# Kernel tuning notes

Measured on AMD Instinct MI355X. Metric: run time of the kernel, lower is better.

Reference implementation:

```python
import jax, jax.numpy as jnp
import numpy as np

B, H, W, C, NH, WS, NB = 8, 64, 64, 384, 12, 8, 2
N = H * W
NWT = WS * WS  # tokens per window
SHIFT = WS // 2

def _rel_index(ws):
    coords = np.stack(np.meshgrid(np.arange(ws), np.arange(ws), indexing='ij')).reshape(2, -1)
    rel = (coords[:, :, None] - coords[:, None, :]).transpose(1, 2, 0)
    rel[..., 0] += ws - 1
    rel[..., 1] += ws - 1
    rel[..., 0] *= 2 * ws - 1
    return rel.sum(-1)  # (ws*ws, ws*ws)

REL_IDX = _rel_index(WS)

def _shift_mask(h, w, ws, shift):
    img = np.zeros((h, w))
    cnt = 0
    for hs in (slice(0, -ws), slice(-ws, -shift), slice(-shift, None)):
        for wsl in (slice(0, -ws), slice(-ws, -shift), slice(-shift, None)):
            img[hs, wsl] = cnt
            cnt += 1
    win = img.reshape(h // ws, ws, w // ws, ws).transpose(0, 2, 1, 3).reshape(-1, ws * ws)
    diff = win[:, None, :] - win[:, :, None]
    return np.where(diff != 0, -100.0, 0.0).astype(np.float32)  # (nW, NWT, NWT)

MASK = jnp.asarray(_shift_mask(H, W, WS, SHIFT))

def _ln(x, g, b, eps=1e-5):
    m = jnp.mean(x, -1, keepdims=True)
    v = jnp.mean((x - m) ** 2, -1, keepdims=True)
    return (x - m) * jax.lax.rsqrt(v + eps) * g + b

def _partition(x):
    b = x.shape[0]
    x = x.reshape(b, H // WS, WS, W // WS, WS, C).transpose(0, 1, 3, 2, 4, 5)
    return x.reshape(-1, NWT, C)

def _reverse(wx, b):
    x = wx.reshape(b, H // WS, W // WS, WS, WS, C).transpose(0, 1, 3, 2, 4, 5)
    return x.reshape(b, H, W, C)

def _attention(xw, qkv_w, qkv_b, proj_w, proj_b, rpb, mask):
    B_, Nt, Cc = xw.shape
    hd = Cc // NH
    qkv = (xw @ qkv_w + qkv_b).reshape(B_, Nt, 3, NH, hd).transpose(2, 0, 3, 1, 4)
    q, k, v = qkv[0], qkv[1], qkv[2]
    bias = rpb[REL_IDX].transpose(2, 0, 1)[None]  # (1, NH, Nt, Nt)
    attn = jnp.einsum('bhnd,bhmd->bhnm', q * (hd ** -0.5), k) + bias
    if mask is not None:
        nW = mask.shape[0]
        attn = attn.reshape(B_ // nW, nW, NH, Nt, Nt) + mask[None, :, None]
        attn = attn.reshape(B_, NH, Nt, Nt)
    attn = jax.nn.softmax(attn, axis=-1)
    out = jnp.einsum('bhnm,bhmd->bhnd', attn, v).transpose(0, 2, 1, 3).reshape(B_, Nt, Cc)
    return out @ proj_w + proj_b

def _swin_block(x, p, shift):
    n1g, n1b, n2g, n2b, qw, qb, pw, pb, w1, b1, w2, b2, rpb = p
    shortcut = x
    h = _ln(x, n1g, n1b)
    if shift > 0:
        h = jnp.roll(h, (-shift, -shift), axis=(1, 2))
    hw = _attention(_partition(h), qw, qb, pw, pb, rpb, MASK if shift > 0 else None)
    h = _reverse(hw, x.shape[0])
    if shift > 0:
        h = jnp.roll(h, (shift, shift), axis=(1, 2))
    x = shortcut + h
    h = _ln(x, n2g, n2b)
    h = jax.nn.gelu(h @ w1 + b1) @ w2 + b2
    return x + h


def setup_inputs() -> dict:
    key = jax.random.key(0)
    ks = jax.random.split(key, 6)
    s = 0.02
    return {
        'x': jax.random.normal(ks[0], (B, N, C), jnp.float32),
        'outer_g': jnp.ones((NB, C), jnp.float32),
        'outer_b': jnp.zeros((NB, C), jnp.float32),
        'n1_g': jnp.ones((NB, C), jnp.float32),
        'n1_b': jnp.zeros((NB, C), jnp.float32),
        'n2_g': jnp.ones((NB, C), jnp.float32),
        'n2_b': jnp.zeros((NB, C), jnp.float32),
        'qkv_w': jax.random.normal(ks[1], (NB, C, 3 * C), jnp.float32) * s,
        'qkv_b': jnp.zeros((NB, 3 * C), jnp.float32),
        'proj_w': jax.random.normal(ks[2], (NB, C, C), jnp.float32) * s,
        'proj_b': jnp.zeros((NB, C), jnp.float32),
        'mlp_w1': jax.random.normal(ks[3], (NB, C, 4 * C), jnp.float32) * s,
        'mlp_b1': jnp.zeros((NB, 4 * C), jnp.float32),
        'mlp_w2': jax.random.normal(ks[4], (NB, 4 * C, C), jnp.float32) * s,
        'mlp_b2': jnp.zeros((NB, C), jnp.float32),
        'rpb': jax.random.normal(ks[5], (NB, (2 * WS - 1) ** 2, NH), jnp.float32) * s,
    }


def reference(x, outer_g, outer_b, n1_g, n1_b, n2_g, n2_b, qkv_w, qkv_b, proj_w, proj_b, mlp_w1, mlp_b1, mlp_w2, mlp_b2, rpb):
    xv = x.reshape(B, H, W, C)
    for i in range(NB):
        shift = 0 if i % 2 == 0 else SHIFT
        p = (n1_g[i], n1_b[i], n2_g[i], n2_b[i], qkv_w[i], qkv_b[i], proj_w[i], proj_b[i],
             mlp_w1[i], mlp_b1[i], mlp_w2[i], mlp_b2[i], rpb[i])
        residual = xv
        xv = _swin_block(_ln(xv, outer_g[i], outer_b[i]), p, shift) + residual
    return xv.reshape(B, N, C)
```

## Files before the change

kernel.cpp:

```cpp
#include <hip/hip_runtime.h>
#include <hip/hip_bf16.h>

#define BATCH 8
#define HDIM 64
#define WDIM 64
#define CC 384
#define NHE 12
#define HD 32
#define NTOK 32768
#define NBLK 2

typedef short short8 __attribute__((ext_vector_type(8)));
typedef float f32x4 __attribute__((ext_vector_type(4)));

__device__ __forceinline__ float bf2f(unsigned short u) {
  return __uint_as_float(((unsigned int)u) << 16);
}
__device__ __forceinline__ unsigned short f2bf(float f) {
  __hip_bfloat16 h = __float2bfloat16(f);
  return *reinterpret_cast<unsigned short*>(&h);
}
__device__ __forceinline__ float wave_sum(float s) {
#pragma unroll
  for (int o = 32; o; o >>= 1) s += __shfl_xor(s, o, 64);
  return s;
}
__device__ __forceinline__ float gelu_f(float x) {
  float y = 0.7978845608028654f * (x + 0.044715f * x * x * x);
  float t = 1.0f - 2.0f / (__expf(2.0f * y) + 1.0f);
  return 0.5f * x * (1.0f + t);
}
__device__ __forceinline__ int regid(int x) {
  return x < 56 ? 0 : (x < 60 ? 1 : 2);
}
__device__ __forceinline__ void gload16(const void* g, void* l) {
  __builtin_amdgcn_global_load_lds(
      (const __attribute__((address_space(1))) unsigned int*)g,
      (__attribute__((address_space(3))) unsigned int*)l, 16, 0, 0);
}

__global__ __launch_bounds__(256) void wconv_all_kernel(
    const float* __restrict__ qkvw, const float* __restrict__ pw,
    const float* __restrict__ w1, const float* __restrict__ w2,
    unsigned short* __restrict__ wt) {
  int t = blockIdx.x;
  const int i = t / 432;
  t -= i * 432;
  unsigned short* wq = wt + (size_t)i * 1769472;
  const float* src;
  unsigned short* dst;
  int K, N, nx;
  if (t < 108)      { src = qkvw + (size_t)i * 442368; dst = wq;           K = 384;  N = 1152; nx = 18; }
  else if (t < 144) { t -= 108; src = pw + (size_t)i * 147456; dst = wq + 442368;  K = 384;  N = 384;  nx = 6; }
  else if (t < 288) { t -= 144; src = w1 + (size_t)i * 589824; dst = wq + 589824;  K = 384;  N = 1536; nx = 24; }
  else              { t -= 288; src = w2 + (size_t)i * 589824; dst = wq + 1179648; K = 1536; N = 384;  nx = 6; }
  const int bn = (t % nx) * 64, bk = (t / nx) * 64;
  __shared__ float tile[64 * 65];
  const int tt = threadIdx.x;
  const int lk = tt >> 2, ln = (tt & 3) * 16;
  const float* ps = src + (size_t)(bk + lk) * N + bn + ln;
#pragma unroll
  for (int j = 0; j < 4; ++j)
    *(float4*)&tile[lk * 65 + ln + 4 * j] = *(const float4*)(ps + 4 * j);
  __syncthreads();
  const int on = tt >> 2, ok = (tt & 3) * 16;
  unsigned short ob[16];
#pragma unroll
  for (int j = 0; j < 16; ++j) ob[j] = f2bf(tile[(ok + j) * 65 + on]);
  uint4* pd = (uint4*)(dst + (size_t)(bn + on) * K + bk + ok);
  pd[0] = ((const uint4*)ob)[0];
  pd[1] = ((const uint4*)ob)[1];
}

__global__ __launch_bounds__(256) void bias_prep_kernel(
    const float* __restrict__ rpb, float* __restrict__ biasT) {
  int idx = blockIdx.x * 256 + threadIdx.x;
  int m = idx & 63;
  int n = (idx >> 6) & 63;
  int h = idx >> 12;
  int dr = (n >> 3) - (m >> 3) + 7;
  int dc = (n & 7) - (m & 7) + 7;
  biasT[idx] = rpb[(dr * 15 + dc) * NHE + h];
}

__global__ __launch_bounds__(256) void ln_fused_kernel(
    const float* __restrict__ xin, const float* __restrict__ og,
    const float* __restrict__ ob, const float* __restrict__ n1g,
    const float* __restrict__ n1b, unsigned short* __restrict__ y0h,
    unsigned short* __restrict__ abuf, int shift) {
  const int lane = threadIdx.x & 63;
  const int token = blockIdx.x * 4 + (threadIdx.x >> 6);
  const float* px = xin + (size_t)token * CC;
  float v[6];
#pragma unroll
  for (int j = 0; j < 6; ++j) v[j] = px[j * 64 + lane];
  float s = 0.f;
#pragma unroll
  for (int j = 0; j < 6; ++j) s += v[j];
  s = wave_sum(s);
  float mean = s * (1.0f / CC);
  float q = 0.f;
#pragma unroll
  for (int j = 0; j < 6; ++j) { float d = v[j] - mean; q += d * d; }
  q = wave_sum(q);
  float rstd = rsqrtf(q * (1.0f / CC) + 1e-5f);
  unsigned short* py = y0h + (size_t)token * CC;
#pragma unroll
  for (int j = 0; j < 6; ++j) {
    int d = j * 64 + lane;
    float y = (v[j] - mean) * rstd * og[d] + ob[d];
    py[d] = f2bf(y);
    v[j] = y;
  }
  s = 0.f;
#pragma unroll
  for (int j = 0; j < 6; ++j) s += v[j];
  s = wave_sum(s);
  float mean2 = s * (1.0f / CC);
  q = 0.f;
#pragma unroll
  for (int j = 0; j < 6; ++j) { float d = v[j] - mean2; q += d * d; }
  q = wave_sum(q);
  float rstd2 = rsqrtf(q * (1.0f / CC) + 1e-5f);
  int b = token >> 12;
  int hh = (token >> 6) & 63;
  int ww = token & 63;
  int r = (hh - shift) & 63;
  int c = (ww - shift) & 63;
  int wrow = (((b << 6) + ((r >> 3) << 3) + (c >> 3)) << 6) + ((r & 7) << 3) + (c & 7);
  unsigned short* pa = abuf + (size_t)wrow * CC;
#pragma unroll
  for (int j = 0; j < 6; ++j) {
    int d = j * 64 + lane;
    pa[d] = f2bf((v[j] - mean2) * rstd2 * n1g[d] + n1b[d]);
  }
}

__global__ __launch_bounds__(256, 2) void apl_kernel(
    const unsigned short* __restrict__ qkv, const float* __restrict__ biasT,
    const unsigned short* __restrict__ y0h, const unsigned short* __restrict__ Btp,
    const float* __restrict__ pb, const float* __restrict__ g2,
    const float* __restrict__ b2, unsigned short* __restrict__ x1h,
    unsigned short* __restrict__ abuf, int shift) {
  __shared__ __align__(1024) char smem[65536];
  const int tid = threadIdx.x;
  const int wv = tid >> 6;
  const int lane = tid & 63;
  const int l0 = lane & 15;
  const int q = lane >> 4;
  const int wi = blockIdx.x;
  const int use_mask = (shift != 0);

  unsigned short* P16 = (unsigned short*)(smem + wv * 12288);
  unsigned short* Vt16 = (unsigned short*)(smem + wv * 12288 + 8192);
  float* Ol = (float*)(smem + wv * 12288);
  unsigned short* Obuf = (unsigned short*)(smem + 49152);

#define LDS_FENCE() asm volatile("s_waitcnt lgkmcnt(0)" ::: "memory")
#define LDS_BARRIER() do { LDS_FENCE(); __builtin_amdgcn_s_barrier(); } while (0)

  f32x4 pacc[4][6] = {};

  for (int p = 0; p < 3; ++p) {
    const int h = 4 * p + wv;
    const unsigned short* qbase = qkv + (size_t)(wi * 64) * 1152 + h * HD;
    short8 kf[4], qf[4];
#pragma unroll
    for (int mt = 0; mt < 4; ++mt)
      kf[mt] = *(const short8*)(qbase + (size_t)(16 * mt + l0) * 1152 + CC + 8 * q);
#pragma unroll
    for (int nt = 0; nt < 4; ++nt)
      qf[nt] = *(const short8*)(qbase + (size_t)(16 * nt + l0) * 1152 + 8 * q);

    f32x4 acc[4][4];
    const float* bh = biasT + h * 4096;
#pragma unroll
    for (int mt = 0; mt < 4; ++mt)
#pragma unroll
      for (int nt = 0; nt < 4; ++nt)
        acc[mt][nt] = *(const f32x4*)(bh + (l0 + 16 * nt) * 64 + 16 * mt + 4 * q);

    {
      unsigned short varr[32];
      const uint4* pv = (const uint4*)(qbase + (size_t)lane * 1152 + 2 * CC);
      uint4* t4 = (uint4*)varr;
      t4[0] = pv[0]; t4[1] = pv[1]; t4[2] = pv[2]; t4[3] = pv[3];
#pragma unroll
      for (int d = 0; d < 32; ++d)
        Vt16[d * 64 + 8 * ((lane >> 3) ^ (d & 7)) + (lane & 7)] = varr[d];
    }

    __builtin_amdgcn_s_setprio(1);
#pragma unroll
    for (int mt = 0; mt < 4; ++mt)
#pragma unroll
      for (int nt = 0; nt < 4; ++nt)
        acc[mt][nt] = __builtin_amdgcn_mfma_f32_16x16x32_bf16(kf[mt], qf[nt], acc[mt][nt], 0, 0, 0);
    __builtin_amdgcn_s_setprio(0);

    if (use_mask) {
      int wloc = wi & 63;
      int wy = (wloc >> 3) * 8, wx = (wloc & 7) * 8;
      int idn[4], idm[16];
#pragma unroll
      for (int nt = 0; nt < 4; ++nt) {
        int n = l0 + 16 * nt;
        idn[nt] = regid(wy + (n >> 3)) * 3 + regid(wx + (n & 7));
      }
#pragma unroll
      for (int mt = 0; mt < 4; ++mt)
#pragma unroll
        for (int r = 0; r < 4; ++r) {
          int m = 16 * mt + 4 * q + r;
          idm[mt * 4 + r] = regid(wy + (m >> 3)) * 3 + regid(wx + (m & 7));
        }
#pragma unroll
      for (int mt = 0; mt < 4; ++mt)
#pragma unroll
        for (int nt = 0; nt < 4; ++nt)
#pragma unroll
          for (int r = 0; r < 4; ++r)
            acc[mt][nt][r] += (idm[mt * 4 + r] == idn[nt]) ? 0.0f : -100.0f;
    }

    float inv[4];
#pragma unroll
    for (int nt = 0; nt < 4; ++nt) {
      float m0 = -1e30f;
#pragma unroll
      for (int mt = 0; mt < 4; ++mt)
#pragma unroll
        for (int r = 0; r < 4; ++r) m0 = fmaxf(m0, acc[mt][nt][r]);
      m0 = fmaxf(m0, __shfl_xor(m0, 16, 64));
      m0 = fmaxf(m0, __shfl_xor(m0, 32, 64));
      float s0 = 0.f;
#pragma unroll
      for (int mt = 0; mt < 4; ++mt)
#pragma unroll
        for (int r = 0; r < 4; ++r) {
          float e = __expf(acc[mt][nt][r] - m0);
          acc[mt][nt][r] = e;
          s0 += e;
        }
      s0 += __shfl_xor(s0, 16, 64);
      s0 += __shfl_xor(s0, 32, 64);
      inv[nt] = 1.0f / s0;
    }

#pragma unroll
    for (int mt = 0; mt < 4; ++mt)
#pragma unroll
      for (int nt = 0; nt < 4; ++nt) {
        unsigned int lo = (unsigned int)f2bf(acc[mt][nt][0] * inv[nt]) |
                          ((unsigned int)f2bf(acc[mt][nt][1] * inv[nt]) << 16);
        unsigned int hi = (unsigned int)f2bf(acc[mt][nt][2] * inv[nt]) |
                          ((unsigned int)f2bf(acc[mt][nt][3] * inv[nt]) << 16);
        unsigned int* dst = (unsigned int*)&P16[(l0 + 16 * nt) * 64 +
                                                8 * ((2 * mt + (q >> 1)) ^ (l0 & 7)) + 4 * (q & 1)];
        dst[0] = lo;
        dst[1] = hi;
      }
    LDS_FENCE();

    f32x4 oacc[4][2] = {};
    __builtin_amdgcn_s_setprio(1);
#pragma unroll
    for (int kt = 0; kt < 2; ++kt) {
      short8 pa[4], vb[2];
#pragma unroll
      for (int nt = 0; nt < 4; ++nt)
        pa[nt] = *(const short8*)&P16[(l0 + 16 * nt) * 64 + 8 * ((q + 4 * kt) ^ (l0 & 7))];
#pragma unroll
      for (int dt = 0; dt < 2; ++dt)
        vb[dt] = *(const short8*)&Vt16[(l0 + 16 * dt) * 64 + 8 * ((q + 4 * kt) ^ (l0 & 7))];
#pragma unroll
      for (int nt = 0; nt < 4; ++nt)
#pragma unroll
        for (int dt = 0; dt < 2; ++dt)
          oacc[nt][dt] = __builtin_amdgcn_mfma_f32_16x16x32_bf16(pa[nt], vb[dt], oacc[nt][dt], 0, 0, 0);
    }
    __builtin_amdgcn_s_setprio(0);
    LDS_FENCE();

#pragma unroll
    for (int nt = 0; nt < 4; ++nt)
#pragma unroll
      for (int dt = 0; dt < 2; ++dt)
#pragma unroll
        for (int r = 0; r < 4; ++r)
          Ol[(16 * nt + 4 * q + r) * 34 + l0 + 16 * dt] = oacc[nt][dt][r];
    LDS_FENCE();

    uint4 opack[4];
    int posv[4];
#pragma unroll
    for (int jj = 0; jj < 4; ++jj) {
      int c = 4 * wv + jj;
      posv[jj] = (c & 8) | ((c ^ lane) & 7);
      unsigned short tmp[8];
#pragma unroll
      for (int e = 0; e < 8; ++e) tmp[e] = f2bf(Ol[lane * 34 + jj * 8 + e]);
      opack[jj] = *(const uint4*)tmp;
    }
    LDS_BARRIER();
#pragma unroll
    for (int jj = 0; jj < 4; ++jj)
      *(uint4*)&Obuf[lane * 128 + posv[jj] * 8] = opack[jj];
    LDS_BARRIER();

#pragma unroll
    for (int kfl = 0; kfl < 4; ++kfl) {
      short8 a[4], b[6];
      int c2 = kfl * 4 + q;
      int pos2 = (c2 & 8) | ((c2 ^ l0) & 7);
#pragma unroll
      for (int mt = 0; mt < 4; ++mt)
        a[mt] = *(const short8*)&Obuf[(16 * mt + l0) * 128 + pos2 * 8];
#pragma unroll
      for (int nt = 0; nt < 6; ++nt)
        b[nt] = *(const short8*)(Btp + (size_t)(wv * 96 + nt * 16 + l0) * 384 +
                                 128 * p + 32 * kfl + 8 * q);
      __builtin_amdgcn_s_setprio(1);
#pragma unroll
      for (int mt = 0; mt < 4; ++mt)
#pragma unroll
        for (int nt = 0; nt < 6; ++nt)
          pacc[mt][nt] = __builtin_amdgcn_mfma_f32_16x16x32_bf16(a[mt], b[nt], pacc[mt][nt], 0, 0, 0);
      __builtin_amdgcn_s_setprio(0);
    }
  }
  LDS_BARRIER();

  float pbv[6], g2v[6], b2v[6];
#pragma unroll
  for (int nt = 0; nt < 6; ++nt) {
    int col = wv * 96 + nt * 16 + l0;
    pbv[nt] = pb[col];
    g2v[nt] = g2[col];
    b2v[nt] = b2[col];
  }
  int dstrow[4][4];
#pragma unroll
  for (int mt = 0; mt < 4; ++mt)
#pragma unroll
    for (int rr = 0; rr < 4; ++rr) {
      int m = 16 * mt + 4 * q + rr;
      int grow = wi * 64 + m;
      int b_ = grow >> 12;
      int wl = (grow >> 6) & 63;
      int t = grow & 63;
      int rs = ((wl >> 3) << 3) + (t >> 3);
      int cs = ((wl & 7) << 3) + (t & 7);
      int hh = (rs + shift) & 63;
      int ww = (cs + shift) & 63;
      dstrow[mt][rr] = (((b_ << 6) + hh) << 6) + ww;
    }
#pragma unroll
  for (int mt = 0; mt < 4; ++mt)
#pragma unroll
    for (int nt = 0; nt < 6; ++nt)
#pragma unroll
      for (int rr = 0; rr < 4; ++rr) {
        size_t dst = (size_t)dstrow[mt][rr] * CC + wv * 96 + nt * 16 + l0;
        pacc[mt][nt][rr] += pbv[nt] + bf2f(y0h[dst]);
      }
  float* part = (float*)(smem + 49152);
  float* stats = (float*)(smem + 49152 + 2048);
#pragma unroll
  for (int mt = 0; mt < 4; ++mt)
#pragma unroll
    for (int rr = 0; rr < 4; ++rr) {
      float s = 0.f, ss = 0.f;
#pragma unroll
      for (int nt = 0; nt < 6; ++nt) {
        float v = pacc[mt][nt][rr];
        s += v;
        ss += v * v;
      }
#pragma unroll
      for (int o = 8; o; o >>= 1) {
        s += __shfl_xor(s, o, 64);
        ss += __shfl_xor(ss, o, 64);
      }
      if (l0 == 0) {
        int m = 16 * mt + 4 * q + rr;
        part[(m * 4 + wv) * 2] = s;
        part[(m * 4 + wv) * 2 + 1] = ss;
      }
    }
  LDS_BARRIER();
  if (tid < 64) {
    float s = 0.f, ss = 0.f;
#pragma unroll
    for (int w = 0; w < 4; ++w) {
      s += part[(tid * 4 + w) * 2];
      ss += part[(tid * 4 + w) * 2 + 1];
    }
    float mean = s * (1.0f / CC);
    float var = ss * (1.0f / CC) - mean * mean;
    stats[tid * 2] = mean;
    stats[tid * 2 + 1] = rsqrtf(var + 1e-5f);
  }
  LDS_BARRIER();
#pragma unroll
  for (int mt = 0; mt < 4; ++mt)
#pragma unroll
    for (int rr = 0; rr < 4; ++rr) {
      int m = 16 * mt + 4 * q + rr;
      float mean = stats[m * 2];
      float rstd = stats[m * 2 + 1];
#pragma unroll
      for (int nt = 0; nt < 6; ++nt) {
        float v = pacc[mt][nt][rr];
        size_t dst = (size_t)dstrow[mt][rr] * CC + wv * 96 + nt * 16 + l0;
        x1h[dst] = f2bf(v);
        abuf[dst] = f2bf((v - mean) * rstd * g2v[nt] + b2v[nt]);
      }
    }
#undef LDS_BARRIER
#undef LDS_FENCE
}

template <int EPI, int NN, int KK>
__global__ __launch_bounds__(256, 2) void gemm_kernel(
    const unsigned short* __restrict__ A, const unsigned short* __restrict__ Bt,
    const float* __restrict__ bias, float* __restrict__ outf,
    unsigned short* __restrict__ outb, const unsigned short* __restrict__ add0h,
    const float* __restrict__ add1f) {
  __shared__ __align__(1024) char smem[65536];
  const int tid = threadIdx.x;
  const int lane = tid & 63;
  const int wv = tid >> 6;
  const int wm = wv & 1, wn = wv >> 1;
  constexpr int NX = NN / 128;
  const int f = blockIdx.y * NX + blockIdx.x;
  const int g = f >> 3;
  const int rowBase = ((f & 7) + 8 * (g / NX)) * 128;
  const int colBase = (g % NX) * 128;
  const int srow = lane >> 3;
  const int schunk = (lane & 7) ^ srow;
  const unsigned short* pA = A + (size_t)(rowBase + srow) * KK + 8 * schunk;
  const unsigned short* pB = Bt + (size_t)(colBase + srow) * KK + 8 * schunk;
  const int l0 = lane & 15;
  const int q = lane >> 4;
  f32x4 acc[4][4] = {};

#pragma unroll
  for (int i = 0; i < 4; ++i) {
    int c = i * 4 + wv;
    gload16(pA + (size_t)(8 * c) * KK, smem + c * 1024);
    gload16(pB + (size_t)(8 * c) * KK, smem + 16384 + c * 1024);
  }

#pragma unroll 2
  for (int k0 = 0; k0 < KK; k0 += 64) {
    const int cur = (k0 >> 6) & 1;
    char* curb = smem + cur * 32768;
    if (k0 + 64 < KK) {
      char* nxtb = smem + (cur ^ 1) * 32768;
#pragma unroll
      for (int i = 0; i < 4; ++i) {
        int c = i * 4 + wv;
        gload16(pA + (size_t)(8 * c) * KK + k0 + 64, nxtb + c * 1024);
        gload16(pB + (size_t)(8 * c) * KK + k0 + 64, nxtb + 16384 + c * 1024);
      }
      asm volatile("s_waitcnt vmcnt(8)" ::: "memory");
    } else {
      asm volatile("s_waitcnt vmcnt(0)" ::: "memory");
    }
    __builtin_amdgcn_s_barrier();
    const unsigned short* As = (const unsigned short*)curb;
    const unsigned short* Bs = (const unsigned short*)(curb + 16384);
#pragma unroll
    for (int ksub = 0; ksub < 2; ++ksub) {
      const int sc = ksub * 4 + q;
      short8 af[4], bfr[4];
#pragma unroll
      for (int im = 0; im < 4; ++im) {
        int r = wm * 64 + im * 16 + l0;
        af[im] = *(const short8*)&As[r * 64 + 8 * (sc ^ (r & 7))];
      }
#pragma unroll
      for (int in_ = 0; in_ < 4; ++in_) {
        int r = wn * 64 + in_ * 16 + l0;
        bfr[in_] = *(const short8*)&Bs[r * 64 + 8 * (sc ^ (r & 7))];
      }
      __builtin_amdgcn_s_setprio(1);
#pragma unroll
      for (int im = 0; im < 4; ++im)
#pragma unroll
        for (int in_ = 0; in_ < 4; ++in_)
          acc[im][in_] = __builtin_amdgcn_mfma_f32_16x16x32_bf16(
              af[im], bfr[in_], acc[im][in_], 0, 0, 0);
      __builtin_amdgcn_s_setprio(0);
    }
    __builtin_amdgcn_s_barrier();
  }
  const int quad = lane >> 4;
  const int lc = lane & 15;
#pragma unroll
  for (int im = 0; im < 4; ++im) {
    int rb = rowBase + wm * 64 + im * 16 + quad * 4;
#pragma unroll
    for (int in_ = 0; in_ < 4; ++in_) {
      int gcol = colBase + wn * 64 + in_ * 16 + lc;
      float bv = bias[gcol];
#pragma unroll
      for (int r = 0; r < 4; ++r) {
        int grow = rb + r;
        float v = acc[im][in_][r] + bv;
        if (EPI == 0) {
          if (gcol < CC) v *= 0.17677669529663687f;
          outb[(size_t)grow * NN + gcol] = f2bf(v);
        } else if (EPI == 1) {
          outb[(size_t)grow * NN + gcol] = f2bf(gelu_f(v));
        } else {
          size_t dst = (size_t)grow * CC + gcol;
          outf[dst] = bf2f(add0h[dst]) + add1f[dst] + v;
        }
      }
    }
  }
}

extern "C" void kernel_launch(void* const* d_in, const int* in_sizes, int n_in,
                              void* d_out, int out_size, void* d_ws, size_t ws_size,
                              hipStream_t stream) {
  const float* x    = (const float*)d_in[0];
  const float* og   = (const float*)d_in[1];
  const float* ob   = (const float*)d_in[2];
  const float* n1g  = (const float*)d_in[3];
  const float* n1b  = (const float*)d_in[4];
  const float* n2g  = (const float*)d_in[5];
  const float* n2b  = (const float*)d_in[6];
  const float* qkvw = (const float*)d_in[7];
  const float* qkvb = (const float*)d_in[8];
  const float* pw   = (const float*)d_in[9];
  const float* pb   = (const float*)d_in[10];
  const float* w1   = (const float*)d_in[11];
  const float* b1   = (const float*)d_in[12];
  const float* w2   = (const float*)d_in[13];
  const float* b2   = (const float*)d_in[14];
  const float* rpb  = (const float*)d_in[15];
  float* out = (float*)d_out;

  char* ws = (char*)d_ws;
  unsigned short* y0h   = (unsigned short*)(ws);
  unsigned short* x1h   = (unsigned short*)(ws + 25165824);
  unsigned short* a_bf  = (unsigned short*)(ws + 50331648);
  unsigned short* big_bf= (unsigned short*)(ws + 100663296);
  unsigned short* wt    = (unsigned short*)(ws + 201326592);
  float* biasT          = (float*)(ws + 100663296 + 75497472);

  wconv_all_kernel<<<864, 256, 0, stream>>>(qkvw, pw, w1, w2, wt);

  for (int i = 0; i < NBLK; ++i) {
    const float* xin = (i == 0) ? x : out;
    int shift = (i & 1) ? 4 : 0;
    unsigned short* wq = wt + (size_t)i * 1769472;
    ln_fused_kernel<<<8192, 256, 0, stream>>>(xin, og + i * 384, ob + i * 384,
                                              n1g + i * 384, n1b + i * 384, y0h, a_bf, shift);
    gemm_kernel<0, 1152, 384><<<dim3(9, 256), 256, 0, stream>>>(
        a_bf, wq, qkvb + i * 1152, nullptr, big_bf, nullptr, nullptr);
    bias_prep_kernel<<<192, 256, 0, stream>>>(rpb + i * 2700, biasT);
    apl_kernel<<<512, 256, 0, stream>>>(big_bf, biasT, y0h, wq + 442368,
                                        pb + i * 384, n2g + i * 384, n2b + i * 384,
                                        x1h, a_bf, shift);
    gemm_kernel<1, 1536, 384><<<dim3(12, 256), 256, 0, stream>>>(
        a_bf, wq + 589824, b1 + i * 1536, nullptr, big_bf, nullptr, nullptr);
    gemm_kernel<3, 384, 1536><<<dim3(3, 256), 256, 0, stream>>>(
        big_bf, wq + 1179648, b2 + i * 384, out, nullptr, x1h, xin);
  }
}
```

Measured before the change: 608.5 us.

## Halve GEMM K-tile to 32 and shrink LDS to raise occupancy

```diff
diff --git a/kernel.cpp b/kernel.cpp
--- a/kernel.cpp
+++ b/kernel.cpp
@@ -422,12 +422,12 @@
 }
 
 template <int EPI, int NN, int KK>
-__global__ __launch_bounds__(256, 2) void gemm_kernel(
+__global__ __launch_bounds__(256, 4) void gemm_kernel(
     const unsigned short* __restrict__ A, const unsigned short* __restrict__ Bt,
     const float* __restrict__ bias, float* __restrict__ outf,
     unsigned short* __restrict__ outb, const unsigned short* __restrict__ add0h,
     const float* __restrict__ add1f) {
-  __shared__ __align__(1024) char smem[65536];
+  __shared__ __align__(1024) char smem[32768];
   const int tid = threadIdx.x;
   const int lane = tid & 63;
   const int wv = tid >> 6;
@@ -437,63 +437,55 @@
   const int g = f >> 3;
   const int rowBase = ((f & 7) + 8 * (g / NX)) * 128;
   const int colBase = (g % NX) * 128;
-  const int srow = lane >> 3;
-  const int schunk = (lane & 7) ^ srow;
+  const int srow = wv * 16 + (lane >> 2);
+  const int schunk = (lane & 3) ^ ((srow >> 1) & 3);
   const unsigned short* pA = A + (size_t)(rowBase + srow) * KK + 8 * schunk;
   const unsigned short* pB = Bt + (size_t)(colBase + srow) * KK + 8 * schunk;
   const int l0 = lane & 15;
   const int q = lane >> 4;
   f32x4 acc[4][4] = {};
 
-#pragma unroll
-  for (int i = 0; i < 4; ++i) {
-    int c = i * 4 + wv;
-    gload16(pA + (size_t)(8 * c) * KK, smem + c * 1024);
-    gload16(pB + (size_t)(8 * c) * KK, smem + 16384 + c * 1024);
-  }
+  gload16(pA, smem + wv * 1024);
+  gload16(pA + (size_t)64 * KK, smem + 4096 + wv * 1024);
+  gload16(pB, smem + 8192 + wv * 1024);
+  gload16(pB + (size_t)64 * KK, smem + 12288 + wv * 1024);
 
 #pragma unroll 2
-  for (int k0 = 0; k0 < KK; k0 += 64) {
-    const int cur = (k0 >> 6) & 1;
-    char* curb = smem + cur * 32768;
-    if (k0 + 64 < KK) {
-      char* nxtb = smem + (cur ^ 1) * 32768;
-#pragma unroll
-      for (int i = 0; i < 4; ++i) {
-        int c = i * 4 + wv;
-        gload16(pA + (size_t)(8 * c) * KK + k0 + 64, nxtb + c * 1024);
-        gload16(pB + (size_t)(8 * c) * KK + k0 + 64, nxtb + 16384 + c * 1024);
-      }
-      asm volatile("s_waitcnt vmcnt(8)" ::: "memory");
+  for (int k0 = 0; k0 < KK; k0 += 32) {
+    const int cur = (k0 >> 5) & 1;
+    char* curb = smem + cur * 16384;
+    if (k0 + 32 < KK) {
+      char* nxtb = smem + (cur ^ 1) * 16384;
+      gload16(pA + k0 + 32, nxtb + wv * 1024);
+      gload16(pA + (size_t)64 * KK + k0 + 32, nxtb + 4096 + wv * 1024);
+      gload16(pB + k0 + 32, nxtb + 8192 + wv * 1024);
+      gload16(pB + (size_t)64 * KK + k0 + 32, nxtb + 12288 + wv * 1024);
+      asm volatile("s_waitcnt vmcnt(4)" ::: "memory");
     } else {
       asm volatile("s_waitcnt vmcnt(0)" ::: "memory");
     }
     __builtin_amdgcn_s_barrier();
     const unsigned short* As = (const unsigned short*)curb;
-    const unsigned short* Bs = (const unsigned short*)(curb + 16384);
-#pragma unroll
-    for (int ksub = 0; ksub < 2; ++ksub) {
-      const int sc = ksub * 4 + q;
-      short8 af[4], bfr[4];
-#pragma unroll
-      for (int im = 0; im < 4; ++im) {
-        int r = wm * 64 + im * 16 + l0;
-        af[im] = *(const short8*)&As[r * 64 + 8 * (sc ^ (r & 7))];
-      }
-#pragma unroll
-      for (int in_ = 0; in_ < 4; ++in_) {
-        int r = wn * 64 + in_ * 16 + l0;
-        bfr[in_] = *(const short8*)&Bs[r * 64 + 8 * (sc ^ (r & 7))];
-      }
-      __builtin_amdgcn_s_setprio(1);
-#pragma unroll
-      for (int im = 0; im < 4; ++im)
-#pragma unroll
-        for (int in_ = 0; in_ < 4; ++in_)
-          acc[im][in_] = __builtin_amdgcn_mfma_f32_16x16x32_bf16(
-              af[im], bfr[in_], acc[im][in_], 0, 0, 0);
-      __builtin_amdgcn_s_setprio(0);
-    }
+    const unsigned short* Bs = (const unsigned short*)(curb + 8192);
+    short8 af[4], bfr[4];
+#pragma unroll
+    for (int im = 0; im < 4; ++im) {
+      int r = wm * 64 + im * 16 + l0;
+      af[im] = *(const short8*)&As[r * 32 + 8 * (q ^ ((r >> 1) & 3))];
+    }
+#pragma unroll
+    for (int in_ = 0; in_ < 4; ++in_) {
+      int r = wn * 64 + in_ * 16 + l0;
+      bfr[in_] = *(const short8*)&Bs[r * 32 + 8 * (q ^ ((r >> 1) & 3))];
+    }
+    __builtin_amdgcn_s_setprio(1);
+#pragma unroll
+    for (int im = 0; im < 4; ++im)
+#pragma unroll
+      for (int in_ = 0; in_ < 4; ++in_)
+        acc[im][in_] = __builtin_amdgcn_mfma_f32_16x16x32_bf16(
+            af[im], bfr[in_], acc[im][in_], 0, 0, 0);
+    __builtin_amdgcn_s_setprio(0);
     __builtin_amdgcn_s_barrier();
   }
   const int quad = lane >> 4;
```

Measured after the change: 630.9 us. +3.7%, slower.

## Fuse MLP fc1, GELU and fc2 into one kernel keeping hidden in LDS

Applied to the files above, without the earlier changes.

```diff
diff --git a/kernel.cpp b/kernel.cpp
--- a/kernel.cpp
+++ b/kernel.cpp
@@ -27,7 +27,7 @@
 }
 __device__ __forceinline__ float gelu_f(float x) {
   float y = 0.7978845608028654f * (x + 0.044715f * x * x * x);
-  float t = 1.0f - 2.0f / (__expf(2.0f * y) + 1.0f);
+  float t = 1.0f - 2.0f * __builtin_amdgcn_rcpf(__expf(2.0f * y) + 1.0f);
   return 0.5f * x * (1.0f + t);
 }
 __device__ __forceinline__ int regid(int x) {
@@ -415,6 +415,118 @@
         size_t dst = (size_t)dstrow[mt][rr] * CC + wv * 96 + nt * 16 + l0;
         x1h[dst] = f2bf(v);
         abuf[dst] = f2bf((v - mean) * rstd * g2v[nt] + b2v[nt]);
+      }
+    }
+#undef LDS_BARRIER
+#undef LDS_FENCE
+}
+
+__global__ __launch_bounds__(256, 1) void mlp_kernel(
+    const unsigned short* __restrict__ A, const unsigned short* __restrict__ w1t,
+    const unsigned short* __restrict__ w2t, const float* __restrict__ b1,
+    const float* __restrict__ b2, const unsigned short* __restrict__ x1h,
+    const float* __restrict__ add1f, float* __restrict__ outf) {
+  __shared__ __align__(1024) char smem[65536];
+  const int tid = threadIdx.x;
+  const int wv = tid >> 6;
+  const int lane = tid & 63;
+  const int l0 = lane & 15;
+  const int q = lane >> 4;
+  const int rowBase = blockIdx.x * 64;
+  float* Ol = (float*)(smem + wv * 12288);
+  unsigned short* Obuf = (unsigned short*)(smem + 49152);
+
+#define LDS_FENCE() asm volatile("s_waitcnt lgkmcnt(0)" ::: "memory")
+#define LDS_BARRIER() do { LDS_FENCE(); __builtin_amdgcn_s_barrier(); } while (0)
+
+  f32x4 pacc[4][6] = {};
+
+  for (int c = 0; c < 12; ++c) {
+    float b1v[2];
+#pragma unroll
+    for (int nt = 0; nt < 2; ++nt)
+      b1v[nt] = b1[c * 128 + wv * 32 + nt * 16 + l0];
+    f32x4 acc2[4][2];
+#pragma unroll
+    for (int mt = 0; mt < 4; ++mt)
+#pragma unroll
+      for (int nt = 0; nt < 2; ++nt) {
+        f32x4 iv = {b1v[nt], b1v[nt], b1v[nt], b1v[nt]};
+        acc2[mt][nt] = iv;
+      }
+#pragma unroll 4
+    for (int ks = 0; ks < 12; ++ks) {
+      short8 af[4], bw[2];
+#pragma unroll
+      for (int mt = 0; mt < 4; ++mt)
+        af[mt] = *(const short8*)(A + (size_t)(rowBase + 16 * mt + l0) * 384 + 32 * ks + 8 * q);
+#pragma unroll
+      for (int nt = 0; nt < 2; ++nt)
+        bw[nt] = *(const short8*)(w1t + (size_t)(c * 128 + wv * 32 + nt * 16 + l0) * 384 + 32 * ks + 8 * q);
+      __builtin_amdgcn_s_setprio(1);
+#pragma unroll
+      for (int mt = 0; mt < 4; ++mt)
+#pragma unroll
+        for (int nt = 0; nt < 2; ++nt)
+          acc2[mt][nt] = __builtin_amdgcn_mfma_f32_16x16x32_bf16(af[mt], bw[nt], acc2[mt][nt], 0, 0, 0);
+      __builtin_amdgcn_s_setprio(0);
+    }
+#pragma unroll
+    for (int mt = 0; mt < 4; ++mt)
+#pragma unroll
+      for (int nt = 0; nt < 2; ++nt)
+#pragma unroll
+        for (int r = 0; r < 4; ++r)
+          Ol[(16 * mt + 4 * q + r) * 34 + l0 + 16 * nt] = gelu_f(acc2[mt][nt][r]);
+    LDS_FENCE();
+    uint4 opack[4];
+    int posv[4];
+#pragma unroll
+    for (int jj = 0; jj < 4; ++jj) {
+      int cc = 4 * wv + jj;
+      posv[jj] = (cc & 8) | ((cc ^ lane) & 7);
+      unsigned short tmp[8];
+#pragma unroll
+      for (int e = 0; e < 8; ++e) tmp[e] = f2bf(Ol[lane * 34 + jj * 8 + e]);
+      opack[jj] = *(const uint4*)tmp;
+    }
+    LDS_BARRIER();
+#pragma unroll
+    for (int jj = 0; jj < 4; ++jj)
+      *(uint4*)&Obuf[lane * 128 + posv[jj] * 8] = opack[jj];
+    LDS_BARRIER();
+#pragma unroll
+    for (int kfl = 0; kfl < 4; ++kfl) {
+      short8 a[4], b[6];
+      int c2 = kfl * 4 + q;
+      int pos2 = (c2 & 8) | ((c2 ^ l0) & 7);
+#pragma unroll
+      for (int mt = 0; mt < 4; ++mt)
+        a[mt] = *(const short8*)&Obuf[(16 * mt + l0) * 128 + pos2 * 8];
+#pragma unroll
+      for (int nt = 0; nt < 6; ++nt)
+        b[nt] = *(const short8*)(w2t + (size_t)(wv * 96 + nt * 16 + l0) * 1536 +
+                                 128 * c + 32 * kfl + 8 * q);
+      __builtin_amdgcn_s_setprio(1);
+#pragma unroll
+      for (int mt = 0; mt < 4; ++mt)
+#pragma unroll
+        for (int nt = 0; nt < 6; ++nt)
+          pacc[mt][nt] = __builtin_amdgcn_mfma_f32_16x16x32_bf16(a[mt], b[nt], pacc[mt][nt], 0, 0, 0);
+      __builtin_amdgcn_s_setprio(0);
+    }
+  }
+#pragma unroll
+  for (int mt = 0; mt < 4; ++mt)
+#pragma unroll
+    for (int nt = 0; nt < 6; ++nt) {
+      int col = wv * 96 + nt * 16 + l0;
+      float bv = b2[col];
+#pragma unroll
+      for (int rr = 0; rr < 4; ++rr) {
+        int row = rowBase + 16 * mt + 4 * q + rr;
+        size_t dst = (size_t)row * CC + col;
+        outf[dst] = pacc[mt][nt][rr] + bv + bf2f(x1h[dst]) + add1f[dst];
       }
     }
 #undef LDS_BARRIER
@@ -566,9 +678,7 @@
     apl_kernel<<<512, 256, 0, stream>>>(big_bf, biasT, y0h, wq + 442368,
                                         pb + i * 384, n2g + i * 384, n2b + i * 384,
                                         x1h, a_bf, shift);
-    gemm_kernel<1, 1536, 384><<<dim3(12, 256), 256, 0, stream>>>(
-        a_bf, wq + 589824, b1 + i * 1536, nullptr, big_bf, nullptr, nullptr);
-    gemm_kernel<3, 384, 1536><<<dim3(3, 256), 256, 0, stream>>>(
-        big_bf, wq + 1179648, b2 + i * 384, out, nullptr, x1h, xin);
-  }
-}
+    mlp_kernel<<<512, 256, 0, stream>>>(a_bf, wq + 589824, wq + 1179648,
+                                        b1 + i * 1536, b2 + i * 384, x1h, xin, out);
+  }
+}
```

New measurement: 990.0 us. 1.63x slower.
